# Kernel tuning notes

Measured on AMD Instinct MI355X. Metric: run time of the kernel, lower is better.

Reference implementation:

```python
import jax, jax.numpy as jnp
import numpy as np

B, T, C, H = 8, 2048, 1024, 64

def setup_inputs() -> dict:
    key = jax.random.key(0)
    ks = jax.random.split(key, 8)
    s = 1.0 / np.sqrt(C)  # ~Linear init scale
    return {
        "x_real": jax.random.normal(ks[0], (B, T, C), jnp.float32),
        "x_imag": jax.random.normal(ks[1], (B, T, C), jnp.float32),
        "Wk_r": jax.random.normal(ks[2], (C, H), jnp.float32) * s,
        "Wk_i": jax.random.normal(ks[3], (C, H), jnp.float32) * s,
        "Wq_r": jax.random.normal(ks[4], (C, H), jnp.float32) * s,
        "Wq_i": jax.random.normal(ks[5], (C, H), jnp.float32) * s,
        "Wv_r": jax.random.normal(ks[6], (C, H), jnp.float32) * s,
        "Wv_i": jax.random.normal(ks[7], (C, H), jnp.float32) * s,
    }

def _complex_linear(x_real, x_imag, Wr, Wi):
    # (xr + i xi) @ (Wr + i Wi)
    out_real = x_real @ Wr - x_imag @ Wi
    out_imag = x_imag @ Wr + x_real @ Wi
    return out_real, out_imag

def reference(x_real, x_imag, Wk_r, Wk_i, Wq_r, Wq_i, Wv_r, Wv_i):
    k_r, k_i = _complex_linear(x_real, x_imag, Wk_r, Wk_i)
    q_r, q_i = _complex_linear(x_real, x_imag, Wq_r, Wq_i)
    v_r, v_i = _complex_linear(x_real, x_imag, Wv_r, Wv_i)
    # complex scores: q @ conj(k)^T equivalent per source math
    wei_real = jnp.einsum('bqh,bkh->bqk', q_r, k_r) + jnp.einsum('bqh,bkh->bqk', q_i, k_i)
    wei_imag = jnp.einsum('bqh,bkh->bqk', q_i, k_r) - jnp.einsum('bqh,bkh->bqk', q_r, k_i)
    eps = 1e-4
    wei_mag = jnp.sqrt(wei_real**2 + wei_imag**2 + eps) * (H ** -0.5)
    causal = jnp.tril(jnp.ones((T, T), dtype=bool))
    wei_mag = jnp.where(causal, wei_mag, -jnp.inf)
    wei = jax.nn.softmax(wei_mag, axis=-1)  # dropout p=0.0 -> identity
    out_real = jnp.einsum('bqk,bkh->bqh', wei, v_r)
    out_imag = jnp.einsum('bqk,bkh->bqh', wei, v_i)
    return out_real, out_imag
```

## Files before the change

### kernel.cpp

```cpp
#include <hip/hip_runtime.h>
#include <hip/hip_bf16.h>
#include <math.h>

#define BB 8
#define TT 2048
#define CC 1024
#define HH 64
#define NROW (BB*TT)
#define NST (NROW*HH)
#define KK2 2048
#define NN 384
#define GN 256
#define VTP 2080

typedef __attribute__((ext_vector_type(8))) short short8;
typedef __attribute__((ext_vector_type(4))) float f32x4;

static __device__ inline unsigned pk_bf16(float a, float b) {
    __hip_bfloat162 h = __float22bfloat162_rn(make_float2(a, b));
    unsigned u; __builtin_memcpy(&u, &h, 4); return u;
}
static __device__ inline short f2bf_s(float a) {
    __hip_bfloat16 h = __float2bfloat16(a);
    short s; __builtin_memcpy(&s, &h, 2); return s;
}
static __device__ inline short8 neg8(short8 a) {
    short8 r;
    #pragma unroll
    for (int i = 0; i < 8; ++i) r[i] = a[i] ^ (short)0x8000;
    return r;
}

static __device__ inline void async16(const void* g, void* l) {
    __builtin_amdgcn_global_load_lds(
        (const __attribute__((address_space(1))) void*)g,
        (__attribute__((address_space(3))) void*)l,
        16, 0, 0);
}

__global__ __launch_bounds__(256) void prep_kernel(
    const float* __restrict__ Wkr, const float* __restrict__ Wki,
    const float* __restrict__ Wqr, const float* __restrict__ Wqi,
    const float* __restrict__ Wvr, const float* __restrict__ Wvi,
    short* __restrict__ Bt)
{
    const int n = blockIdx.x;
    const int g = n >> 6, h = n & 63;
    const int p = g >> 1;
    const bool im = g & 1;
    const float* Wr = (p == 0) ? Wkr : (p == 1) ? Wqr : Wvr;
    const float* Wi = (p == 0) ? Wki : (p == 1) ? Wqi : Wvi;
    const float* W1 = im ? Wi : Wr;
    const float* W2 = im ? Wr : Wi;
    const float s2 = im ? 1.f : -1.f;

    #pragma unroll
    for (int j = 0; j < 8; ++j) {
        int k = threadIdx.x + 256 * j;
        float v = (k < CC) ? W1[k * HH + h] : s2 * W2[(k - CC) * HH + h];
        Bt[(size_t)n * KK2 + k] = f2bf_s(v);
    }
}

__global__ __launch_bounds__(256) void convert_x(
    const float* __restrict__ xr, const float* __restrict__ xi,
    short* __restrict__ X)
{
    int v = blockIdx.x * 256 + threadIdx.x;
    #pragma unroll
    for (int it = 0; it < 4; ++it, v += 4096 * 256) {
        int row = v >> 8;
        int c8 = v & 255;
        const float* src = (c8 < 128) ? xr : xi;
        int col = (c8 & 127) * 8;
        const float4* p = (const float4*)&src[(size_t)row * CC + col];
        float4 a = p[0], b = p[1];
        uint4 o;
        o.x = pk_bf16(a.x, a.y);
        o.y = pk_bf16(a.z, a.w);
        o.z = pk_bf16(b.x, b.y);
        o.w = pk_bf16(b.z, b.w);
        *(uint4*)&X[(size_t)row * KK2 + c8 * 8] = o;
    }
}

#define LDP 72
#define STP 136

__global__ __launch_bounds__(256) void proj_gemm(
    const short* __restrict__ X,
    const short* __restrict__ Bt,
    short* __restrict__ G, short* __restrict__ VT)
{
    __shared__ __attribute__((aligned(16))) short sAB[128 * 64 + 64 * 64];
    short* sA = sAB;
    short* sB = sAB + 128 * 64;

    const int tid = threadIdx.x;
    const int mbase = blockIdx.x * 128;
    const int comp = blockIdx.y;

    const int wave = tid >> 6, lane = tid & 63;
    const int wr = wave >> 1, wc = wave & 1;
    const int quad = lane >> 4, lm = lane & 15;

    const int lgrp = lane >> 3;
    const int lslot = lane & 7;
    const int scol = ((lslot ^ lgrp) << 4);

    const char* Ag = (const char*)(X + (size_t)mbase * KK2);
    const char* Bg = (const char*)(Bt + (size_t)comp * 64 * KK2);

    f32x4 acc[4][2] = {};

    for (int ks = 0; ks < KK2 / 64; ++ks) {
        #pragma unroll
        for (int i = 0; i < 4; ++i) {
            int q = wave * 4 + i;
            async16(Ag + (size_t)(q * 8 + lgrp) * (KK2 * 2) + ks * 128 + scol,
                    (char*)sA + q * 1024);
        }
        #pragma unroll
        for (int i = 0; i < 2; ++i) {
            int q = wave * 2 + i;
            async16(Bg + (size_t)(q * 8 + lgrp) * (KK2 * 2) + ks * 128 + scol,
                    (char*)sB + q * 1024);
        }
        __syncthreads();

        #pragma unroll
        for (int kk = 0; kk < 2; ++kk) {
            const int cs = (kk * 32 + quad * 8) ^ ((lm & 7) << 3);
            short8 af[4], bf[2];
            #pragma unroll
            for (int mi = 0; mi < 4; ++mi)
                af[mi] = *(const short8*)&sA[(64 * wr + 16 * mi + lm) * 64 + cs];
            #pragma unroll
            for (int ni = 0; ni < 2; ++ni)
                bf[ni] = *(const short8*)&sB[(32 * wc + 16 * ni + lm) * 64 + cs];
            #pragma unroll
            for (int mi = 0; mi < 4; ++mi)
                #pragma unroll
                for (int ni = 0; ni < 2; ++ni)
                    acc[mi][ni] = __builtin_amdgcn_mfma_f32_16x16x32_bf16(
                        af[mi], bf[ni], acc[mi][ni], 0, 0, 0);
        }
        __syncthreads();
    }

    if (comp < 4) {
        short* sG = sAB;
        #pragma unroll
        for (int mi = 0; mi < 4; ++mi)
            #pragma unroll
            for (int ni = 0; ni < 2; ++ni)
                #pragma unroll
                for (int r = 0; r < 4; ++r)
                    sG[(64*wr + 16*mi + quad*4 + r) * LDP + 32*wc + 16*ni + lm] =
                        f2bf_s(acc[mi][ni][r]);
        __syncthreads();
        #pragma unroll
        for (int j = 0; j < 4; ++j) {
            int id = tid + 256 * j;
            int row = id >> 3, c8 = id & 7;
            uint4 v = *(const uint4*)&sG[row * LDP + c8 * 8];
            *(uint4*)&G[(size_t)(mbase + row) * GN + comp*64 + c8*8] = v;
        }
    } else {
        short* sT = sAB;
        const int vcomp = comp - 4;
        const int b = mbase >> 11;
        const int tb = mbase & 2047;
        #pragma unroll
        for (int mi = 0; mi < 4; ++mi)
            #pragma unroll
            for (int ni = 0; ni < 2; ++ni)
                #pragma unroll
                for (int r = 0; r < 4; ++r)
                    sT[(32*wc + 16*ni + lm) * STP + 64*wr + 16*mi + quad*4 + r] =
                        f2bf_s(acc[mi][ni][r]);
        __syncthreads();
        #pragma unroll
        for (int j = 0; j < 4; ++j) {
            int id = tid + 256 * j;
            int h = id >> 4, c = id & 15;
            uint4 v = *(const uint4*)&sT[h * STP + c * 8];
            *(uint4*)&VT[(((size_t)vcomp*BB + b)*64 + h)*VTP + tb + c*8] = v;
        }
    }
}

#define PLDS 72

__global__ __launch_bounds__(256) void attn_kernel(
    const short* __restrict__ G,
    const short* __restrict__ VT,
    float* __restrict__ out)
{
    __shared__ float comb[4][16][128];
    __shared__ float cmw[4][16], clw[4][16];

    const int tid = threadIdx.x;
    const int wave = tid >> 6, lane = tid & 63;
    const int quad = lane >> 4, lm = lane & 15;
    const int j = (int)(gridDim.x - 1) - (int)blockIdx.x;
    const int b = blockIdx.y;
    const int qbase = j * 16;
    const int nkt = (j >> 2) + 1;

    const short* Qrow = G + ((size_t)(b*TT + qbase + lm)) * GN + 128;
    short8 A1[4], A2[4];
    #pragma unroll
    for (int ks = 0; ks < 4; ++ks)
        A1[ks] = *(const short8*)(Qrow + ks*32 + quad*8);
    A2[0] = A1[2]; A2[1] = A1[3];
    A2[2] = neg8(A1[0]); A2[3] = neg8(A1[1]);

    f32x4 Or[4], Oi[4];
    #pragma unroll
    for (int h = 0; h < 4; ++h)
        #pragma unroll
        for (int r = 0; r < 4; ++r) { Or[h][r] = 0.f; Oi[h][r] = 0.f; }
    float m[4], l[4];
    #pragma unroll
    for (int r = 0; r < 4; ++r) { m[r] = -INFINITY; l[r] = 0.f; }

    short* Pw = (short*)&comb[wave][0][0];
    const short* Vrb = VT + (size_t)b * 64 * VTP;
    const short* Vib = VT + ((size_t)BB + b) * 64 * VTP;

    for (int kt = wave; kt < nkt; kt += 4) {
        const int kb = kt * 64;
        const short* Kt = G + ((size_t)(b*TT + kb)) * GN;

        f32x4 mag[4];
        #pragma unroll
        for (int nt = 0; nt < 4; ++nt) {
            const short* Krow = Kt + (size_t)(nt*16 + lm) * GN;
            short8 Bf[4];
            #pragma unroll
            for (int ks = 0; ks < 4; ++ks)
                Bf[ks] = *(const short8*)(Krow + ks*32 + quad*8);
            f32x4 sr = {0.f,0.f,0.f,0.f}, si = {0.f,0.f,0.f,0.f};
            #pragma unroll
            for (int ks = 0; ks < 4; ++ks) {
                sr = __builtin_amdgcn_mfma_f32_16x16x32_bf16(A1[ks], Bf[ks], sr, 0,0,0);
                si = __builtin_amdgcn_mfma_f32_16x16x32_bf16(A2[ks], Bf[ks], si, 0,0,0);
            }
            int tok = kb + nt*16 + lm;
            #pragma unroll
            for (int r = 0; r < 4; ++r) {
                float v = sqrtf(fmaf(sr[r], sr[r], fmaf(si[r], si[r], 1e-4f))) * 0.125f;
                int qrow = qbase + quad*4 + r;
                mag[nt][r] = (tok > qrow) ? -INFINITY : v;
            }
        }

        float tm[4];
        #pragma unroll
        for (int r = 0; r < 4; ++r)
            tm[r] = fmaxf(fmaxf(mag[0][r], mag[1][r]), fmaxf(mag[2][r], mag[3][r]));
        #pragma unroll
        for (int d = 1; d < 16; d <<= 1)
            #pragma unroll
            for (int r = 0; r < 4; ++r)
                tm[r] = fmaxf(tm[r], __shfl_xor(tm[r], d, 16));

        float al[4], ps[4];
        #pragma unroll
        for (int r = 0; r < 4; ++r) {
            float mn = fmaxf(m[r], tm[r]);
            al[r] = __expf(m[r] - mn);
            m[r] = mn;
            ps[r] = 0.f;
        }
        #pragma unroll
        for (int nt = 0; nt < 4; ++nt)
            #pragma unroll
            for (int r = 0; r < 4; ++r) {
                float p = __expf(mag[nt][r] - m[r]);
                mag[nt][r] = p;
                ps[r] += p;
            }
        #pragma unroll
        for (int d = 1; d < 16; d <<= 1)
            #pragma unroll
            for (int r = 0; r < 4; ++r)
                ps[r] += __shfl_xor(ps[r], d, 16);
        #pragma unroll
        for (int r = 0; r < 4; ++r)
            l[r] = fmaf(l[r], al[r], ps[r]);

        #pragma unroll
        for (int h = 0; h < 4; ++h)
            #pragma unroll
            for (int r = 0; r < 4; ++r) { Or[h][r] *= al[r]; Oi[h][r] *= al[r]; }

        #pragma unroll
        for (int nt = 0; nt < 4; ++nt)
            #pragma unroll
            for (int r = 0; r < 4; ++r)
                Pw[(quad*4 + r) * PLDS + nt*16 + lm] = f2bf_s(mag[nt][r]);
        short8 Af0 = *(const short8*)&Pw[lm * PLDS + quad*8];
        short8 Af1 = *(const short8*)&Pw[lm * PLDS + 32 + quad*8];

        #pragma unroll
        for (int ht = 0; ht < 4; ++ht) {
            const short* vr0 = Vrb + (size_t)(ht*16 + lm) * VTP + kb + quad*8;
            const short* vi0 = Vib + (size_t)(ht*16 + lm) * VTP + kb + quad*8;
            short8 br0 = *(const short8*)(vr0);
            short8 br1 = *(const short8*)(vr0 + 32);
            short8 bi0 = *(const short8*)(vi0);
            short8 bi1 = *(const short8*)(vi0 + 32);
            Or[ht] = __builtin_amdgcn_mfma_f32_16x16x32_bf16(Af0, br0, Or[ht], 0,0,0);
            Or[ht] = __builtin_amdgcn_mfma_f32_16x16x32_bf16(Af1, br1, Or[ht], 0,0,0);
            Oi[ht] = __builtin_amdgcn_mfma_f32_16x16x32_bf16(Af0, bi0, Oi[ht], 0,0,0);
            Oi[ht] = __builtin_amdgcn_mfma_f32_16x16x32_bf16(Af1, bi1, Oi[ht], 0,0,0);
        }
    }

    __syncthreads();

    #pragma unroll
    for (int ht = 0; ht < 4; ++ht)
        #pragma unroll
        for (int r = 0; r < 4; ++r) {
            comb[wave][quad*4 + r][ht*16 + lm]      = Or[ht][r];
            comb[wave][quad*4 + r][64 + ht*16 + lm] = Oi[ht][r];
        }
    if (lm == 0) {
        #pragma unroll
        for (int r = 0; r < 4; ++r) {
            cmw[wave][quad*4 + r] = m[r];
            clw[wave][quad*4 + r] = l[r];
        }
    }
    __syncthreads();

    for (int e = tid; e < 16*128; e += 256) {
        int q = e >> 7, h = e & 127;
        float mstar = fmaxf(fmaxf(cmw[0][q], cmw[1][q]), fmaxf(cmw[2][q], cmw[3][q]));
        float osum = 0.f, lsum = 0.f;
        #pragma unroll
        for (int w = 0; w < 4; ++w) {
            float f = __expf(cmw[w][q] - mstar);
            osum = fmaf(f, comb[w][q][h], osum);
            lsum = fmaf(f, clw[w][q], lsum);
        }
        float res = osum / lsum;
        int comp = h >> 6, hh = h & 63;
        out[(size_t)comp * NST + ((size_t)(b*TT + qbase + q)) * HH + hh] = res;
    }
}

extern "C" void kernel_launch(void* const* d_in, const int* in_sizes, int n_in,
                              void* d_out, int out_size, void* d_ws, size_t ws_size,
                              hipStream_t stream)
{
    const float* xr  = (const float*)d_in[0];
    const float* xi  = (const float*)d_in[1];
    const float* Wkr = (const float*)d_in[2];
    const float* Wki = (const float*)d_in[3];
    const float* Wqr = (const float*)d_in[4];
    const float* Wqi = (const float*)d_in[5];
    const float* Wvr = (const float*)d_in[6];
    const float* Wvi = (const float*)d_in[7];

    short* Bt = (short*)d_ws;
    short* G  = (short*)((char*)d_ws + (2u  << 20));
    short* VT = (short*)((char*)d_ws + (11u << 20));
    short* X  = (short*)((char*)d_ws + (16u << 20));
    float* out = (float*)d_out;

    prep_kernel<<<NN, 256, 0, stream>>>(Wkr, Wki, Wqr, Wqi, Wvr, Wvi, Bt);

    convert_x<<<4096, 256, 0, stream>>>(xr, xi, X);

    dim3 g1(NROW / 128, 6);
    proj_gemm<<<g1, 256, 0, stream>>>(X, Bt, G, VT);

    dim3 g3(TT / 16, BB);
    attn_kernel<<<g3, 256, 0, stream>>>(G, VT, out);
}
```

Measured before the change: 294.6 us.

## Use exp2 softmax, lazy rescaling, MFMA row sums, and MFMA priority hints

Folds log2(e) into the score scale so the softmax uses native exp2 and hardware sqrt. The running max is only updated, and the accumulators rescaled, when a tile's max exceeds it by more than 8, which drops the per-tile rescale in the common case. The row-sum shuffle reduction is replaced by an MFMA against a ones vector, which sums the bf16 probabilities. s_setprio wraps the MFMA blocks to favour issue among waves. The trade-off is some softmax-normalisation precision: the row sum now uses rounded bf16 probabilities, and values can grow by up to 2^8 before a rescale.

Measured after the change: 282.8 us. 4.0% less time.

```diff
diff --git a/kernel.cpp b/kernel.cpp
--- a/kernel.cpp
+++ b/kernel.cpp
@@ -191,6 +191,7 @@
 }
 
 #define PLDS 72
+#define SC2 0.18033688f
 
 __global__ __launch_bounds__(256) void attn_kernel(
     const short* __restrict__ G,
@@ -216,14 +217,19 @@
     A2[0] = A1[2]; A2[1] = A1[3];
     A2[2] = neg8(A1[0]); A2[3] = neg8(A1[1]);
 
+    short8 ones;
+    #pragma unroll
+    for (int i = 0; i < 8; ++i) ones[i] = (short)0x3F80;
+
     f32x4 Or[4], Oi[4];
     #pragma unroll
     for (int h = 0; h < 4; ++h)
         #pragma unroll
         for (int r = 0; r < 4; ++r) { Or[h][r] = 0.f; Oi[h][r] = 0.f; }
-    float m[4], l[4];
-    #pragma unroll
-    for (int r = 0; r < 4; ++r) { m[r] = -INFINITY; l[r] = 0.f; }
+    f32x4 Ol = {0.f, 0.f, 0.f, 0.f};
+    float m[4];
+    #pragma unroll
+    for (int r = 0; r < 4; ++r) m[r] = -INFINITY;
 
     short* Pw = (short*)&comb[wave][0][0];
     const short* Vrb = VT + (size_t)b * 64 * VTP;
@@ -242,15 +248,18 @@
             for (int ks = 0; ks < 4; ++ks)
                 Bf[ks] = *(const short8*)(Krow + ks*32 + quad*8);
             f32x4 sr = {0.f,0.f,0.f,0.f}, si = {0.f,0.f,0.f,0.f};
+            __builtin_amdgcn_s_setprio(1);
             #pragma unroll
             for (int ks = 0; ks < 4; ++ks) {
                 sr = __builtin_amdgcn_mfma_f32_16x16x32_bf16(A1[ks], Bf[ks], sr, 0,0,0);
                 si = __builtin_amdgcn_mfma_f32_16x16x32_bf16(A2[ks], Bf[ks], si, 0,0,0);
             }
+            __builtin_amdgcn_s_setprio(0);
             int tok = kb + nt*16 + lm;
             #pragma unroll
             for (int r = 0; r < 4; ++r) {
-                float v = sqrtf(fmaf(sr[r], sr[r], fmaf(si[r], si[r], 1e-4f))) * 0.125f;
+                float v = __builtin_amdgcn_sqrtf(
+                              fmaf(sr[r], sr[r], fmaf(si[r], si[r], 1e-4f))) * SC2;
                 int qrow = qbase + quad*4 + r;
                 mag[nt][r] = (tok > qrow) ? -INFINITY : v;
             }
@@ -266,43 +275,38 @@
             for (int r = 0; r < 4; ++r)
                 tm[r] = fmaxf(tm[r], __shfl_xor(tm[r], d, 16));
 
-        float al[4], ps[4];
-        #pragma unroll
-        for (int r = 0; r < 4; ++r) {
-            float mn = fmaxf(m[r], tm[r]);
-            al[r] = __expf(m[r] - mn);
-            m[r] = mn;
-            ps[r] = 0.f;
-        }
+        int need = (tm[0] > m[0] + 8.f) | (tm[1] > m[1] + 8.f) |
+                   (tm[2] > m[2] + 8.f) | (tm[3] > m[3] + 8.f);
+        if (__any(need)) {
+            float al[4];
+            #pragma unroll
+            for (int r = 0; r < 4; ++r) {
+                float mn = fmaxf(m[r], tm[r]);
+                al[r] = __builtin_amdgcn_exp2f(m[r] - mn);
+                m[r] = mn;
+            }
+            #pragma unroll
+            for (int h = 0; h < 4; ++h)
+                #pragma unroll
+                for (int r = 0; r < 4; ++r) { Or[h][r] *= al[r]; Oi[h][r] *= al[r]; }
+            #pragma unroll
+            for (int r = 0; r < 4; ++r) Ol[r] *= al[r];
+        }
+
         #pragma unroll
         for (int nt = 0; nt < 4; ++nt)
             #pragma unroll
             for (int r = 0; r < 4; ++r) {
-                float p = __expf(mag[nt][r] - m[r]);
-                mag[nt][r] = p;
-                ps[r] += p;
+                float p = __builtin_amdgcn_exp2f(mag[nt][r] - m[r]);
+                Pw[(quad*4 + r) * PLDS + nt*16 + lm] = f2bf_s(p);
             }
-        #pragma unroll
-        for (int d = 1; d < 16; d <<= 1)
-            #pragma unroll
-            for (int r = 0; r < 4; ++r)
-                ps[r] += __shfl_xor(ps[r], d, 16);
-        #pragma unroll
-        for (int r = 0; r < 4; ++r)
-            l[r] = fmaf(l[r], al[r], ps[r]);
-
-        #pragma unroll
-        for (int h = 0; h < 4; ++h)
-            #pragma unroll
-            for (int r = 0; r < 4; ++r) { Or[h][r] *= al[r]; Oi[h][r] *= al[r]; }
-
-        #pragma unroll
-        for (int nt = 0; nt < 4; ++nt)
-            #pragma unroll
-            for (int r = 0; r < 4; ++r)
-                Pw[(quad*4 + r) * PLDS + nt*16 + lm] = f2bf_s(mag[nt][r]);
         short8 Af0 = *(const short8*)&Pw[lm * PLDS + quad*8];
         short8 Af1 = *(const short8*)&Pw[lm * PLDS + 32 + quad*8];
+
+        __builtin_amdgcn_s_setprio(1);
+        Ol = __builtin_amdgcn_mfma_f32_16x16x32_bf16(Af0, ones, Ol, 0,0,0);
+        Ol = __builtin_amdgcn_mfma_f32_16x16x32_bf16(Af1, ones, Ol, 0,0,0);
+        __builtin_amdgcn_s_setprio(0);
 
         #pragma unroll
         for (int ht = 0; ht < 4; ++ht) {
@@ -312,10 +316,12 @@
             short8 br1 = *(const short8*)(vr0 + 32);
             short8 bi0 = *(const short8*)(vi0);
             short8 bi1 = *(const short8*)(vi0 + 32);
+            __builtin_amdgcn_s_setprio(1);
             Or[ht] = __builtin_amdgcn_mfma_f32_16x16x32_bf16(Af0, br0, Or[ht], 0,0,0);
             Or[ht] = __builtin_amdgcn_mfma_f32_16x16x32_bf16(Af1, br1, Or[ht], 0,0,0);
             Oi[ht] = __builtin_amdgcn_mfma_f32_16x16x32_bf16(Af0, bi0, Oi[ht], 0,0,0);
             Oi[ht] = __builtin_amdgcn_mfma_f32_16x16x32_bf16(Af1, bi1, Oi[ht], 0,0,0);
+            __builtin_amdgcn_s_setprio(0);
         }
     }
 
@@ -332,7 +338,7 @@
         #pragma unroll
         for (int r = 0; r < 4; ++r) {
             cmw[wave][quad*4 + r] = m[r];
-            clw[wave][quad*4 + r] = l[r];
+            clw[wave][quad*4 + r] = Ol[r];
         }
     }
     __syncthreads();
@@ -343,7 +349,7 @@
         float osum = 0.f, lsum = 0.f;
         #pragma unroll
         for (int w = 0; w < 4; ++w) {
-            float f = __expf(cmw[w][q] - mstar);
+            float f = __builtin_amdgcn_exp2f(cmw[w][q] - mstar);
             osum = fmaf(f, comb[w][q][h], osum);
             lsum = fmaf(f, clw[w][q], lsum);
         }
```
